# Kernel tuning notes

Measured on AMD Instinct MI355X. Metric: run time of the kernel, lower is better.

The kernel has to match this reference:

```python
import jax, jax.numpy as jnp
import numpy as np

B, D, H, C, HALT_H, MAX_STEPS = 8192, 2048, 1024, 1000, 32, 10
EPS = 1e-08


def setup_inputs() -> dict:
    key = jax.random.key(0)
    ks = jax.random.split(key, 12)
    s = 0.02
    return {
        "x": jax.random.normal(ks[0], (B, D), jnp.float32),
        "enc_W": jax.random.normal(ks[1], (H, D), jnp.float32) * s,
        "enc_b": jnp.zeros((H,), jnp.float32),
        "ln_g": jnp.ones((H,), jnp.float32),
        "ln_b": jnp.zeros((H,), jnp.float32),
        "W_ih": jax.random.normal(ks[2], (3 * H, H), jnp.float32) * s,
        "W_hh": jax.random.normal(ks[3], (3 * H, H), jnp.float32) * s,
        "b_ih": jnp.zeros((3 * H,), jnp.float32),
        "b_hh": jnp.zeros((3 * H,), jnp.float32),
        "cls_W": jax.random.normal(ks[4], (C, H), jnp.float32) * s,
        "cls_b": jnp.zeros((C,), jnp.float32),
        "h1_W": jax.random.normal(ks[5], (HALT_H, H), jnp.float32) * s,
        "h1_b": jnp.zeros((HALT_H,), jnp.float32),
        "h2_W": jax.random.normal(ks[6], (1, HALT_H), jnp.float32) * s,
        "h2_b": jnp.zeros((1,), jnp.float32),
    }


def _forward(x, enc_W, enc_b, ln_g, ln_b, W_ih, W_hh, b_ih, b_hh,
             cls_W, cls_b, h1_W, h1_b, h2_W, h2_b):
    # encoder: Linear -> LayerNorm -> GELU (exact)
    z = x @ enc_W.T + enc_b
    mu = jnp.mean(z, axis=-1, keepdims=True)
    var = jnp.var(z, axis=-1, keepdims=True)
    z = (z - mu) * jax.lax.rsqrt(var + 1e-05) * ln_g + ln_b
    h0 = jax.nn.gelu(z, approximate=False)

    def step(h, _):
        gi = h @ W_ih.T + b_ih   # GRUCell with input = hidden
        gh = h @ W_hh.T + b_hh
        gi_r, gi_z, gi_n = jnp.split(gi, 3, axis=-1)
        gh_r, gh_z, gh_n = jnp.split(gh, 3, axis=-1)
        r = jax.nn.sigmoid(gi_r + gh_r)
        zt = jax.nn.sigmoid(gi_z + gh_z)
        n = jnp.tanh(gi_n + r * gh_n)
        h_new = (1.0 - zt) * n + zt * h
        logits = h_new @ cls_W.T + cls_b                         # [B, C]
        halt = jax.nn.sigmoid(
            jax.nn.relu(h_new @ h1_W.T + h1_b) @ h2_W.T + h2_b
        )[:, 0]                                                   # [B]
        return h_new, (logits, halt)

    _, (logits_steps, halt_steps) = jax.lax.scan(step, h0, None, length=MAX_STEPS)
    logits_stack = jnp.transpose(logits_steps, (1, 0, 2))  # [B, T, C]
    halts_stack = jnp.transpose(halt_steps, (1, 0))        # [B, T]

    log_not_halt = jnp.log(1.0 - halts_stack + EPS)
    cumsum_log = jnp.cumsum(log_not_halt, axis=1)
    cumsum_shifted = jnp.concatenate(
        [jnp.zeros((halts_stack.shape[0], 1), halts_stack.dtype), cumsum_log[:, :-1]], axis=1)
    halt_dist = halts_stack * jnp.exp(cumsum_shifted)
    remainder = 1.0 - jnp.sum(halt_dist, axis=1, keepdims=True)
    halt_dist = jnp.concatenate(
        [halt_dist[:, :-1], halt_dist[:, -1:] + jnp.maximum(remainder, 0.0)], axis=1)

    weighted_logits = jnp.sum(halt_dist[:, :, None] * logits_stack, axis=1)  # [B, C]
    step_indices = jnp.arange(1, MAX_STEPS + 1, dtype=weighted_logits.dtype)
    expected_steps = jnp.sum(halt_dist * step_indices, axis=1)
    probs = jax.nn.softmax(weighted_logits, axis=1)
    softmax_conf = jnp.max(probs, axis=1)
    comp_uncertainty = expected_steps / MAX_STEPS
    confidence = 0.7 * softmax_conf + 0.3 * (1.0 - comp_uncertainty)
    return (weighted_logits, probs, confidence, softmax_conf,
            expected_steps, halt_dist, comp_uncertainty)


def reference(x, enc_W, enc_b, ln_g, ln_b, W_ih, W_hh, b_ih, b_hh,
              cls_W, cls_b, h1_W, h1_b, h2_W, h2_b):
    return _forward(x, enc_W, enc_b, ln_g, ln_b, W_ih, W_hh, b_ih, b_hh,
                    cls_W, cls_b, h1_W, h1_b, h2_W, h2_b)
```

## Files before the change

### kernel.cpp

```cpp
#include <hip/hip_runtime.h>
#include <hip/hip_bf16.h>

#define B_ 8192
#define D_ 2048
#define H_ 1024
#define C_ 1000
#define NSTEP 10

typedef __attribute__((ext_vector_type(8))) short short8;
typedef __attribute__((ext_vector_type(4))) float f32x4;

__device__ __forceinline__ f32x4 mfma16x16(short8 a, short8 b, f32x4 c) {
  return __builtin_amdgcn_mfma_f32_16x16x32_bf16(a, b, c, 0, 0, 0);
}

__device__ __forceinline__ void async16(void* lds_uniform, const void* gsrc) {
  __builtin_amdgcn_global_load_lds(
      (const __attribute__((address_space(1))) void*)gsrc,
      (__attribute__((address_space(3))) void*)lds_uniform, 16, 0, 0);
}

__device__ __forceinline__ float sigm(float x) { return 1.0f / (1.0f + __expf(-x)); }
__device__ __forceinline__ float tanh_fast(float x) { return 1.0f - 2.0f / (__expf(2.0f * x) + 1.0f); }
__device__ __forceinline__ float b2f(short s) {
  union { unsigned u; float f; } v; v.u = ((unsigned)(unsigned short)s) << 16; return v.f;
}
__device__ __forceinline__ unsigned short f2us(float f) {
  __hip_bfloat16 h = __float2bfloat16(f); return *(unsigned short*)&h;
}

__device__ __forceinline__ int swz(int row, int slot) {
  return (row << 7) + (((slot) ^ (row & 7)) << 4);
}

__global__ void cvt_bf16_pad(const float* __restrict__ src, __hip_bfloat16* __restrict__ dst,
                             int n4, int nsrc4) {
  int i = blockIdx.x * 256 + threadIdx.x;
  if (i >= n4) return;
  float4 v = make_float4(0.f, 0.f, 0.f, 0.f);
  if (i < nsrc4) v = ((const float4*)src)[i];
  ((ushort4*)dst)[i] = make_ushort4(f2us(v.x), f2us(v.y), f2us(v.z), f2us(v.w));
}

__global__ void cvt_gates(const float* __restrict__ Wih, const float* __restrict__ Whh,
                          __hip_bfloat16* __restrict__ dst) {
  const int i = blockIdx.x * 256 + threadIdx.x;
  const int per_gate = (H_ * H_) / 4;
  const int gate = i / per_gate, rem = i - gate * per_gate;
  float4 v;
  if (gate == 0) {
    float4 a = ((const float4*)Wih)[rem], b = ((const float4*)Whh)[rem];
    v = make_float4(a.x + b.x, a.y + b.y, a.z + b.z, a.w + b.w);
  } else if (gate == 1) {
    float4 a = ((const float4*)Wih)[per_gate + rem], b = ((const float4*)Whh)[per_gate + rem];
    v = make_float4(a.x + b.x, a.y + b.y, a.z + b.z, a.w + b.w);
  } else if (gate == 2) {
    v = ((const float4*)Wih)[2 * per_gate + rem];
  } else {
    v = ((const float4*)Whh)[2 * per_gate + rem];
  }
  ((ushort4*)dst)[i] = make_ushort4(f2us(v.x), f2us(v.y), f2us(v.z), f2us(v.w));
}

template<int EPI>
__global__ __launch_bounds__(256, 2)
void gemm_bt(const __hip_bfloat16* __restrict__ A, int lda,
             const __hip_bfloat16* __restrict__ Bt, int ldb, int K,
             const float* __restrict__ bias,
             float* __restrict__ out, int out_ld, int ncol,
             const float* __restrict__ wrow) {
  __shared__ __hip_bfloat16 sA[128 * 64];
  __shared__ __hip_bfloat16 sB[128 * 64];
  const int tid = threadIdx.x;
  const int wave = tid >> 6, lane = tid & 63;
  const int m0 = blockIdx.x * 128, n0 = blockIdx.y * 128;
  const int wm = (wave >> 1) * 64, wn = (wave & 1) * 64;
  const int lr = lane & 15;
  const int g4 = lane >> 4;
  const int srow = wave * 8 + (lane >> 3);
  const int scol = ((lane & 7) ^ ((lane >> 3) & 7)) * 8;

  f32x4 acc[4][4] = {};

  const __hip_bfloat16* Asrc = A + (size_t)(m0 + srow) * lda + scol;
  const __hip_bfloat16* Bsrc = Bt + (size_t)(n0 + srow) * ldb + scol;

  for (int k0 = 0; k0 < K; k0 += 64) {
#pragma unroll
    for (int c = 0; c < 4; ++c) {
      async16((char*)sA + c * 4096 + wave * 1024, Asrc + (size_t)(c * 32) * lda + k0);
      async16((char*)sB + c * 4096 + wave * 1024, Bsrc + (size_t)(c * 32) * ldb + k0);
    }
    __syncthreads();
#pragma unroll
    for (int ks = 0; ks < 2; ++ks) {
      const int slot = ks * 4 + g4;
      short8 af[4], bfr[4];
#pragma unroll
      for (int i = 0; i < 4; ++i) {
        af[i]  = *(const short8*)((const char*)sA + swz(wm + i * 16 + lr, slot));
        bfr[i] = *(const short8*)((const char*)sB + swz(wn + i * 16 + lr, slot));
      }
#pragma unroll
      for (int i = 0; i < 4; ++i)
#pragma unroll
        for (int j = 0; j < 4; ++j)
          acc[i][j] = mfma16x16(af[i], bfr[j], acc[i][j]);
    }
    __syncthreads();
  }

  const int rbase = (lane >> 4) * 4;
  const int cbase = lane & 15;
#pragma unroll
  for (int i = 0; i < 4; ++i) {
#pragma unroll
    for (int r = 0; r < 4; ++r) {
      const int grow = m0 + wm + i * 16 + rbase + r;
      if (EPI == 1) {
        const float ws = wrow[grow];
#pragma unroll
        for (int j = 0; j < 4; ++j) {
          const int gcol = n0 + wn + j * 16 + cbase;
          if (gcol < ncol)
            out[(size_t)grow * out_ld + gcol] = acc[i][j][r] + bias[gcol] * ws;
        }
      } else {
#pragma unroll
        for (int j = 0; j < 4; ++j) {
          const int gcol = n0 + wn + j * 16 + cbase;
          out[(size_t)grow * out_ld + gcol] = acc[i][j][r] + bias[gcol];
        }
      }
    }
  }
}

__global__ __launch_bounds__(256, 2)
void gemm_gru(const __hip_bfloat16* __restrict__ A,
              const __hip_bfloat16* __restrict__ Wc4,
              const float* __restrict__ b_ih, const float* __restrict__ b_hh,
              __hip_bfloat16* __restrict__ hnewb) {
  __shared__ __hip_bfloat16 sA[128 * 64];
  __shared__ __hip_bfloat16 sB[4 * 64 * 64];
  const int tid = threadIdx.x, wave = tid >> 6, lane = tid & 63;
  const int m0 = blockIdx.x * 128, n0 = blockIdx.y * 64;
  const int wr = wave >> 1, wc = wave & 1;
  const int lr = lane & 15;
  const int g4 = lane >> 4;
  const int srow = lane >> 3;
  const int scol = ((lane & 7) ^ ((lane >> 3) & 7)) * 8;

  f32x4 acc[4][4][2] = {};

  const __hip_bfloat16* Asrc = A + (size_t)(m0 + wave * 8 + srow) * H_ + scol;
  const __hip_bfloat16* Bsrc = Wc4 + (size_t)(n0 + wave * 8 + srow) * H_ + scol;

  for (int k0 = 0; k0 < H_; k0 += 64) {
#pragma unroll
    for (int c = 0; c < 4; ++c)
      async16((char*)sA + c * 4096 + wave * 1024, Asrc + (size_t)(c * 32) * H_ + k0);
#pragma unroll
    for (int g = 0; g < 4; ++g)
#pragma unroll
      for (int d = 0; d < 2; ++d)
        async16((char*)sB + g * 8192 + d * 4096 + wave * 1024,
                Bsrc + ((size_t)g << 20) + (size_t)(d * 32) * H_ + k0);
    __syncthreads();
#pragma unroll
    for (int ks = 0; ks < 2; ++ks) {
      const int slot = ks * 4 + g4;
      short8 af[4];
#pragma unroll
      for (int mi = 0; mi < 4; ++mi)
        af[mi] = *(const short8*)((const char*)sA + swz(wr * 64 + mi * 16 + lr, slot));
      short8 bf[4][2];
#pragma unroll
      for (int g = 0; g < 4; ++g)
#pragma unroll
        for (int hb = 0; hb < 2; ++hb)
          bf[g][hb] = *(const short8*)((const char*)sB + g * 8192
                                       + swz(wc * 32 + hb * 16 + lr, slot));
#pragma unroll
      for (int mi = 0; mi < 4; ++mi)
#pragma unroll
        for (int g = 0; g < 4; ++g)
#pragma unroll
          for (int hb = 0; hb < 2; ++hb)
            acc[mi][g][hb] = mfma16x16(af[mi], bf[g][hb], acc[mi][g][hb]);
    }
    __syncthreads();
  }

  const int rbase = (lane >> 4) * 4;
  const int cbase = lane & 15;
#pragma unroll
  for (int hb = 0; hb < 2; ++hb) {
    const int gcol = n0 + wc * 32 + hb * 16 + cbase;
    const float brz = b_ih[gcol] + b_hh[gcol];
    const float bzz = b_ih[H_ + gcol] + b_hh[H_ + gcol];
    const float bin = b_ih[2 * H_ + gcol];
    const float bhn = b_hh[2 * H_ + gcol];
#pragma unroll
    for (int mi = 0; mi < 4; ++mi) {
#pragma unroll
      for (int r = 0; r < 4; ++r) {
        const int grow = m0 + wr * 64 + mi * 16 + rbase + r;
        const size_t idx = (size_t)grow * H_ + gcol;
        const float rg = sigm(acc[mi][0][hb][r] + brz);
        const float zg = sigm(acc[mi][1][hb][r] + bzz);
        const float ng = tanh_fast(acc[mi][2][hb][r] + bin + rg * (acc[mi][3][hb][r] + bhn));
        const float hv = b2f(*(const short*)(A + idx));
        hnewb[idx] = __float2bfloat16((1.0f - zg) * ng + zg * hv);
      }
    }
  }
}

__global__ void ln_gelu(const float* __restrict__ z, const float* __restrict__ g,
                        const float* __restrict__ bta, __hip_bfloat16* __restrict__ hb) {
  const int row = blockIdx.x, t = threadIdx.x;
  __shared__ float rs[4], rs2[4];
  float4 v = ((const float4*)(z + (size_t)row * H_))[t];
  float s = v.x + v.y + v.z + v.w;
  float s2 = v.x * v.x + v.y * v.y + v.z * v.z + v.w * v.w;
#pragma unroll
  for (int off = 32; off; off >>= 1) {
    s += __shfl_down(s, off);
    s2 += __shfl_down(s2, off);
  }
  if ((t & 63) == 0) { rs[t >> 6] = s; rs2[t >> 6] = s2; }
  __syncthreads();
  const float mu = (rs[0] + rs[1] + rs[2] + rs[3]) * (1.0f / H_);
  const float var = (rs2[0] + rs2[1] + rs2[2] + rs2[3]) * (1.0f / H_) - mu * mu;
  const float rstd = rsqrtf(var + 1e-5f);
  float4 gg = ((const float4*)g)[t];
  float4 bb = ((const float4*)bta)[t];
  float o[4], res[4];
  o[0] = (v.x - mu) * rstd * gg.x + bb.x;
  o[1] = (v.y - mu) * rstd * gg.y + bb.y;
  o[2] = (v.z - mu) * rstd * gg.z + bb.z;
  o[3] = (v.w - mu) * rstd * gg.w + bb.w;
#pragma unroll
  for (int k = 0; k < 4; ++k)
    res[k] = 0.5f * o[k] * (1.0f + erff(o[k] * 0.70710678118654752f));
  ((ushort4*)(hb + (size_t)row * H_))[t] =
      make_ushort4(f2us(res[0]), f2us(res[1]), f2us(res[2]), f2us(res[3]));
}

__global__ __launch_bounds__(256, 4)
void halt_mlp_all(const __hip_bfloat16* __restrict__ hstack,
                  const __hip_bfloat16* __restrict__ h1Wb,
                  const float* __restrict__ h1b, const float* __restrict__ h2W,
                  const float* __restrict__ h2b,
                  float* __restrict__ hbuf) {
  __shared__ float part[2][2][64][8];
  const int tid = threadIdx.x, wave = tid >> 6, lane = tid & 63;
  const int tstep = blockIdx.y;
  const __hip_bfloat16* hb = hstack + (size_t)(tstep + 1) * B_ * H_;
  const int rowgrp = wave >> 1, khalf = wave & 1;
  const int m0 = (blockIdx.x * 2 + rowgrp) * 16;
  const int lr = lane & 15, lk = (lane >> 4) * 8;

  const __hip_bfloat16* Arow = hb + (size_t)(m0 + lr) * H_ + khalf * 512 + lk;
  const __hip_bfloat16* B0 = h1Wb + (size_t)lr * H_ + khalf * 512 + lk;
  const __hip_bfloat16* B1 = h1Wb + (size_t)(16 + lr) * H_ + khalf * 512 + lk;
  f32x4 acc0 = {}, acc1 = {};
#pragma unroll 4
  for (int kk = 0; kk < 512; kk += 32) {
    short8 a  = *(const short8*)(Arow + kk);
    short8 b0 = *(const short8*)(B0 + kk);
    short8 b1 = *(const short8*)(B1 + kk);
    acc0 = mfma16x16(a, b0, acc0);
    acc1 = mfma16x16(a, b1, acc1);
  }
#pragma unroll
  for (int q = 0; q < 4; ++q) {
    part[rowgrp][khalf][lane][q]     = acc0[q];
    part[rowgrp][khalf][lane][4 + q] = acc1[q];
  }
  __syncthreads();
  if (khalf) return;

  const float w2a = h2W[lr], w2b = h2W[16 + lr];
  const float b1a = h1b[lr], b1b = h1b[16 + lr];
  float p[4];
#pragma unroll
  for (int q = 0; q < 4; ++q) {
    const float u0 = part[rowgrp][0][lane][q]     + part[rowgrp][1][lane][q]     + b1a;
    const float u1 = part[rowgrp][0][lane][4 + q] + part[rowgrp][1][lane][4 + q] + b1b;
    p[q] = fmaxf(u0, 0.f) * w2a + fmaxf(u1, 0.f) * w2b;
  }
#pragma unroll
  for (int m = 1; m < 16; m <<= 1) {
#pragma unroll
    for (int q = 0; q < 4; ++q) p[q] += __shfl_xor(p[q], m);
  }
  if (lr == 0) {
    const float b2 = h2b[0];
#pragma unroll
    for (int q = 0; q < 4; ++q) {
      const int row = m0 + (lane >> 4) * 4 + q;
      hbuf[(size_t)row * NSTEP + tstep] = 1.f / (1.f + expf(-(p[q] + b2)));
    }
  }
}

__global__ void ponder_rec(const float* __restrict__ hbuf,
                           float* __restrict__ out_hd, float* __restrict__ out_es,
                           float* __restrict__ out_cu, float* __restrict__ wsum) {
  const int row = blockIdx.x * 256 + threadIdx.x;
  const float* hp = hbuf + (size_t)row * NSTEP;
  float c = 0.f, ps = 0.f, es = 0.f;
  float hd[NSTEP];
#pragma unroll
  for (int t = 0; t < NSTEP; ++t) {
    const float halt = hp[t];
    const float pt = halt * expf(c);
    float w;
    if (t == NSTEP - 1) {
      w = pt + fmaxf(1.f - (ps + pt), 0.f);
    } else {
      w = pt;
      c += logf(1.f - halt + 1e-8f);
      ps += pt;
    }
    es += w * (float)(t + 1);
    hd[t] = w;
  }
#pragma unroll
  for (int t = 0; t < NSTEP; ++t) out_hd[(size_t)row * NSTEP + t] = hd[t];
  out_es[row] = es;
  out_cu[row] = es * (1.0f / NSTEP);
  wsum[row] = ps + hd[NSTEP - 1];
}

__global__ void hw_final(const __hip_bfloat16* __restrict__ hstack,
                         const float* __restrict__ out_hd,
                         __hip_bfloat16* __restrict__ hwb) {
  const int t = threadIdx.x;
  const int row = blockIdx.x * 4 + (t >> 6);
  const int c0 = (t & 63) * 16;
  const float* hd = out_hd + (size_t)row * NSTEP;
  float accv[16] = {};
#pragma unroll
  for (int s = 0; s < NSTEP; ++s) {
    const float w = hd[s];
    const short8* p = (const short8*)(hstack + ((size_t)(s + 1) * B_ + row) * H_ + c0);
    short8 a0 = p[0], a1 = p[1];
#pragma unroll
    for (int q = 0; q < 8; ++q) accv[q] += w * b2f(a0[q]);
#pragma unroll
    for (int q = 0; q < 8; ++q) accv[8 + q] += w * b2f(a1[q]);
  }
  short8 r0, r1;
#pragma unroll
  for (int q = 0; q < 8; ++q) { r0[q] = (short)f2us(accv[q]); r1[q] = (short)f2us(accv[8 + q]); }
  short8* dst = (short8*)(hwb + (size_t)row * H_ + c0);
  dst[0] = r0; dst[1] = r1;
}

__global__ void finalize(const float* __restrict__ wl, const float* __restrict__ es,
                         float* __restrict__ probs, float* __restrict__ conf,
                         float* __restrict__ sconf) {
  const int row = blockIdx.x, t = threadIdx.x;
  __shared__ float red[4], red2[4];
  float4 v = make_float4(-1e30f, -1e30f, -1e30f, -1e30f);
  float m = -1e30f;
  if (t < 250) {
    v = ((const float4*)(wl + (size_t)row * C_))[t];
    m = fmaxf(fmaxf(v.x, v.y), fmaxf(v.z, v.w));
  }
#pragma unroll
  for (int off = 32; off; off >>= 1) m = fmaxf(m, __shfl_down(m, off));
  if ((t & 63) == 0) red[t >> 6] = m;
  __syncthreads();
  m = fmaxf(fmaxf(red[0], red[1]), fmaxf(red[2], red[3]));
  float4 e = make_float4(0.f, 0.f, 0.f, 0.f);
  float s = 0.f;
  if (t < 250) {
    e.x = expf(v.x - m); e.y = expf(v.y - m); e.z = expf(v.z - m); e.w = expf(v.w - m);
    s = e.x + e.y + e.z + e.w;
  }
#pragma unroll
  for (int off = 32; off; off >>= 1) s += __shfl_down(s, off);
  if ((t & 63) == 0) red2[t >> 6] = s;
  __syncthreads();
  s = red2[0] + red2[1] + red2[2] + red2[3];
  const float inv = 1.0f / s;
  if (t < 250)
    ((float4*)(probs + (size_t)row * C_))[t] = make_float4(e.x * inv, e.y * inv, e.z * inv, e.w * inv);
  if (t == 0) {
    sconf[row] = inv;
    conf[row] = 0.7f * inv + 0.3f * (1.0f - es[row] * (1.0f / NSTEP));
  }
}

extern "C" void kernel_launch(void* const* d_in, const int* in_sizes, int n_in,
                              void* d_out, int out_size, void* d_ws, size_t ws_size,
                              hipStream_t stream) {
  (void)in_sizes; (void)n_in; (void)out_size; (void)ws_size;
  const float* x     = (const float*)d_in[0];
  const float* enc_W = (const float*)d_in[1];
  const float* enc_b = (const float*)d_in[2];
  const float* ln_g  = (const float*)d_in[3];
  const float* ln_b  = (const float*)d_in[4];
  const float* W_ih  = (const float*)d_in[5];
  const float* W_hh  = (const float*)d_in[6];
  const float* b_ih  = (const float*)d_in[7];
  const float* b_hh  = (const float*)d_in[8];
  const float* cls_W = (const float*)d_in[9];
  const float* cls_b = (const float*)d_in[10];
  const float* h1_W  = (const float*)d_in[11];
  const float* h1_b  = (const float*)d_in[12];
  const float* h2_W  = (const float*)d_in[13];
  const float* h2_b  = (const float*)d_in[14];

  char* wsp = (char*)d_ws;
  auto carve = [&](size_t n) { char* p = wsp; wsp += (n + 255) & ~(size_t)255; return p; };
  __hip_bfloat16* Wc4b   = (__hip_bfloat16*)carve((size_t)4 * H_ * H_ * 2);
  __hip_bfloat16* clsWb  = (__hip_bfloat16*)carve((size_t)1024 * 1024 * 2);
  __hip_bfloat16* encWb  = (__hip_bfloat16*)carve((size_t)H_ * D_ * 2);
  __hip_bfloat16* h1Wb   = (__hip_bfloat16*)carve((size_t)32 * H_ * 2);
  __hip_bfloat16* hstack = (__hip_bfloat16*)carve((size_t)(NSTEP + 1) * B_ * H_ * 2);
  float* wsum = (float*)carve((size_t)B_ * 4);
  float* hbuf = (float*)carve((size_t)B_ * NSTEP * 4);

  const size_t SLOT = (size_t)B_ * H_;
  float* z            = (float*)(hstack + SLOT);
  __hip_bfloat16* xb  = hstack + 3 * SLOT;
  __hip_bfloat16* hwb = hstack;

  float* out = (float*)d_out;
  float* out_wl    = out;
  float* out_probs = out + (size_t)B_ * C_;
  float* out_conf  = out + (size_t)2 * B_ * C_;
  float* out_sconf = out_conf + B_;
  float* out_es    = out_sconf + B_;
  float* out_hd    = out_es + B_;
  float* out_cu    = out_hd + (size_t)B_ * NSTEP;

  dim3 blk(256);
  { int n4 = B_ * D_ / 4;       cvt_bf16_pad<<<(n4 + 255) / 256, blk, 0, stream>>>(x, xb, n4, n4); }
  { int n4 = H_ * D_ / 4;       cvt_bf16_pad<<<(n4 + 255) / 256, blk, 0, stream>>>(enc_W, encWb, n4, n4); }
  { int n4 = 4 * H_ * H_ / 4;   cvt_gates<<<(n4 + 255) / 256, blk, 0, stream>>>(W_ih, W_hh, Wc4b); }
  { int n4 = 1024 * 1024 / 4;   cvt_bf16_pad<<<(n4 + 255) / 256, blk, 0, stream>>>(cls_W, clsWb, n4, C_ * H_ / 4); }
  { int n4 = 32 * H_ / 4;       cvt_bf16_pad<<<(n4 + 255) / 256, blk, 0, stream>>>(h1_W, h1Wb, n4, n4); }

  gemm_bt<0><<<dim3(B_ / 128, H_ / 128), blk, 0, stream>>>(
      xb, D_, encWb, D_, D_, enc_b, z, H_, H_, nullptr);
  ln_gelu<<<B_, blk, 0, stream>>>(z, ln_g, ln_b, hstack);

  for (int step = 0; step < NSTEP; ++step) {
    const __hip_bfloat16* hprev = hstack + (size_t)step * SLOT;
    __hip_bfloat16* hnext = hstack + (size_t)(step + 1) * SLOT;
    gemm_gru<<<dim3(B_ / 128, H_ / 64), blk, 0, stream>>>(
        hprev, Wc4b, b_ih, b_hh, hnext);
  }

  halt_mlp_all<<<dim3(B_ / 32, NSTEP), blk, 0, stream>>>(
      hstack, h1Wb, h1_b, h2_W, h2_b, hbuf);
  ponder_rec<<<B_ / 256, blk, 0, stream>>>(hbuf, out_hd, out_es, out_cu, wsum);

  hw_final<<<B_ / 4, blk, 0, stream>>>(hstack, out_hd, hwb);

  gemm_bt<1><<<dim3(B_ / 128, 1024 / 128), blk, 0, stream>>>(
      hwb, H_, clsWb, H_, H_, cls_b, out_wl, C_, C_, wsum);

  finalize<<<B_, blk, 0, stream>>>(out_wl, out_es, out_probs, out_conf, out_sconf);
}
```

Measured before the change: 907.5 us.

## Overlap halt MLP with GRU steps and merge weight conversion kernels

The halting MLP for step t-1 now runs inside the GRU kernel for step t, using an extra grid column (blockIdx.y==16) that reads the previous hidden state. Only the final step needs a separate halt_last kernel. The five fp32-to-bf16 conversion launches are merged into one cvt_all kernel that dispatches on the flat index. The aim is to hide the halt MLP's memory reads behind GRU GEMM work and to cut launch overhead, at the cost of a slightly uneven grid and extra branching.

```diff
diff --git a/kernel.cpp b/kernel.cpp
--- a/kernel.cpp
+++ b/kernel.cpp
@@ -33,33 +33,108 @@
   return (row << 7) + (((slot) ^ (row & 7)) << 4);
 }
 
-__global__ void cvt_bf16_pad(const float* __restrict__ src, __hip_bfloat16* __restrict__ dst,
-                             int n4, int nsrc4) {
-  int i = blockIdx.x * 256 + threadIdx.x;
-  if (i >= n4) return;
-  float4 v = make_float4(0.f, 0.f, 0.f, 0.f);
-  if (i < nsrc4) v = ((const float4*)src)[i];
-  ((ushort4*)dst)[i] = make_ushort4(f2us(v.x), f2us(v.y), f2us(v.z), f2us(v.w));
-}
-
-__global__ void cvt_gates(const float* __restrict__ Wih, const float* __restrict__ Whh,
-                          __hip_bfloat16* __restrict__ dst) {
+__device__ __forceinline__ void halt_rows32(
+    const __hip_bfloat16* __restrict__ hb, const __hip_bfloat16* __restrict__ h1Wb,
+    const float* __restrict__ h1b, const float* __restrict__ h2W,
+    const float* __restrict__ h2b, float* __restrict__ hbuf, int tcol,
+    int m0base, float (*part)[2][64][8]) {
+  const int tid = threadIdx.x, wave = tid >> 6, lane = tid & 63;
+  const int rowgrp = wave >> 1, khalf = wave & 1;
+  const int m0 = m0base + rowgrp * 16;
+  const int lr = lane & 15, lk = (lane >> 4) * 8;
+
+  const __hip_bfloat16* Arow = hb + (size_t)(m0 + lr) * H_ + khalf * 512 + lk;
+  const __hip_bfloat16* B0 = h1Wb + (size_t)lr * H_ + khalf * 512 + lk;
+  const __hip_bfloat16* B1 = h1Wb + (size_t)(16 + lr) * H_ + khalf * 512 + lk;
+  f32x4 acc0 = {}, acc1 = {};
+#pragma unroll 4
+  for (int kk = 0; kk < 512; kk += 32) {
+    short8 a  = *(const short8*)(Arow + kk);
+    short8 b0 = *(const short8*)(B0 + kk);
+    short8 b1 = *(const short8*)(B1 + kk);
+    acc0 = mfma16x16(a, b0, acc0);
+    acc1 = mfma16x16(a, b1, acc1);
+  }
+#pragma unroll
+  for (int q = 0; q < 4; ++q) {
+    part[rowgrp][khalf][lane][q]     = acc0[q];
+    part[rowgrp][khalf][lane][4 + q] = acc1[q];
+  }
+  __syncthreads();
+  if (!khalf) {
+    const float w2a = h2W[lr], w2b = h2W[16 + lr];
+    const float b1a = h1b[lr], b1b = h1b[16 + lr];
+    float p[4];
+#pragma unroll
+    for (int q = 0; q < 4; ++q) {
+      const float u0 = part[rowgrp][0][lane][q]     + part[rowgrp][1][lane][q]     + b1a;
+      const float u1 = part[rowgrp][0][lane][4 + q] + part[rowgrp][1][lane][4 + q] + b1b;
+      p[q] = fmaxf(u0, 0.f) * w2a + fmaxf(u1, 0.f) * w2b;
+    }
+#pragma unroll
+    for (int m = 1; m < 16; m <<= 1) {
+#pragma unroll
+      for (int q = 0; q < 4; ++q) p[q] += __shfl_xor(p[q], m);
+    }
+    if (lr == 0) {
+      const float b2 = h2b[0];
+#pragma unroll
+      for (int q = 0; q < 4; ++q) {
+        const int row = m0 + (lane >> 4) * 4 + q;
+        hbuf[(size_t)row * NSTEP + tcol] = 1.f / (1.f + expf(-(p[q] + b2)));
+      }
+    }
+  }
+  __syncthreads();
+}
+
+__global__ void cvt_all(const float* __restrict__ x, const float* __restrict__ encW,
+                        const float* __restrict__ Wih, const float* __restrict__ Whh,
+                        const float* __restrict__ clsW, const float* __restrict__ h1W,
+                        __hip_bfloat16* __restrict__ xb, __hip_bfloat16* __restrict__ encWb,
+                        __hip_bfloat16* __restrict__ Wc4b, __hip_bfloat16* __restrict__ clsWb,
+                        __hip_bfloat16* __restrict__ h1Wb) {
   const int i = blockIdx.x * 256 + threadIdx.x;
-  const int per_gate = (H_ * H_) / 4;
-  const int gate = i / per_gate, rem = i - gate * per_gate;
+  const int b0 = B_ * D_ / 4;
+  const int b1 = b0 + H_ * D_ / 4;
+  const int b2 = b1 + H_ * H_;
+  const int b3 = b2 + 1024 * 1024 / 4;
+  const int b4 = b3 + 32 * H_ / 4;
+  if (i >= b4) return;
   float4 v;
-  if (gate == 0) {
-    float4 a = ((const float4*)Wih)[rem], b = ((const float4*)Whh)[rem];
-    v = make_float4(a.x + b.x, a.y + b.y, a.z + b.z, a.w + b.w);
-  } else if (gate == 1) {
-    float4 a = ((const float4*)Wih)[per_gate + rem], b = ((const float4*)Whh)[per_gate + rem];
-    v = make_float4(a.x + b.x, a.y + b.y, a.z + b.z, a.w + b.w);
-  } else if (gate == 2) {
-    v = ((const float4*)Wih)[2 * per_gate + rem];
+  __hip_bfloat16* dst;
+  int di;
+  if (i < b0) {
+    v = ((const float4*)x)[i]; dst = xb; di = i;
+  } else if (i < b1) {
+    const int j = i - b0;
+    v = ((const float4*)encW)[j]; dst = encWb; di = j;
+  } else if (i < b2) {
+    const int j = i - b1;
+    const int per_gate = H_ * H_ / 4;
+    const int gate = j / per_gate, rem = j - gate * per_gate;
+    if (gate == 0) {
+      float4 a = ((const float4*)Wih)[rem], b = ((const float4*)Whh)[rem];
+      v = make_float4(a.x + b.x, a.y + b.y, a.z + b.z, a.w + b.w);
+    } else if (gate == 1) {
+      float4 a = ((const float4*)Wih)[per_gate + rem], b = ((const float4*)Whh)[per_gate + rem];
+      v = make_float4(a.x + b.x, a.y + b.y, a.z + b.z, a.w + b.w);
+    } else if (gate == 2) {
+      v = ((const float4*)Wih)[2 * per_gate + rem];
+    } else {
+      v = ((const float4*)Whh)[2 * per_gate + rem];
+    }
+    dst = Wc4b; di = j;
+  } else if (i < b3) {
+    const int j = i - b2;
+    v = make_float4(0.f, 0.f, 0.f, 0.f);
+    if (j < C_ * H_ / 4) v = ((const float4*)clsW)[j];
+    dst = clsWb; di = j;
   } else {
-    v = ((const float4*)Whh)[2 * per_gate + rem];
-  }
-  ((ushort4*)dst)[i] = make_ushort4(f2us(v.x), f2us(v.y), f2us(v.z), f2us(v.w));
+    const int j = i - b3;
+    v = ((const float4*)h1W)[j]; dst = h1Wb; di = j;
+  }
+  ((ushort4*)dst)[di] = make_ushort4(f2us(v.x), f2us(v.y), f2us(v.z), f2us(v.w));
 }
 
 template<int EPI>
@@ -140,9 +215,22 @@
 void gemm_gru(const __hip_bfloat16* __restrict__ A,
               const __hip_bfloat16* __restrict__ Wc4,
               const float* __restrict__ b_ih, const float* __restrict__ b_hh,
-              __hip_bfloat16* __restrict__ hnewb) {
+              __hip_bfloat16* __restrict__ hnewb,
+              const __hip_bfloat16* __restrict__ h1Wb,
+              const float* __restrict__ h1b, const float* __restrict__ h2W,
+              const float* __restrict__ h2b, float* __restrict__ hbuf, int tcol) {
   __shared__ __hip_bfloat16 sA[128 * 64];
   __shared__ __hip_bfloat16 sB[4 * 64 * 64];
+  if (blockIdx.y == 16) {
+    if (tcol >= 0) {
+      float (*part)[2][64][8] = (float (*)[2][64][8])sA;
+      const int band = blockIdx.x * 128;
+#pragma unroll
+      for (int c = 0; c < 4; ++c)
+        halt_rows32(A, h1Wb, h1b, h2W, h2b, hbuf, tcol, band + c * 32, part);
+    }
+    return;
+  }
   const int tid = threadIdx.x, wave = tid >> 6, lane = tid & 63;
   const int m0 = blockIdx.x * 128, n0 = blockIdx.y * 64;
   const int wr = wave >> 1, wc = wave & 1;
@@ -215,6 +303,15 @@
       }
     }
   }
+}
+
+__global__ __launch_bounds__(256, 4)
+void halt_last(const __hip_bfloat16* __restrict__ hb,
+               const __hip_bfloat16* __restrict__ h1Wb,
+               const float* __restrict__ h1b, const float* __restrict__ h2W,
+               const float* __restrict__ h2b, float* __restrict__ hbuf, int tcol) {
+  __shared__ float part[2][2][64][8];
+  halt_rows32(hb, h1Wb, h1b, h2W, h2b, hbuf, tcol, blockIdx.x * 32, part);
 }
 
 __global__ void ln_gelu(const float* __restrict__ z, const float* __restrict__ g,
@@ -246,64 +343,6 @@
     res[k] = 0.5f * o[k] * (1.0f + erff(o[k] * 0.70710678118654752f));
   ((ushort4*)(hb + (size_t)row * H_))[t] =
       make_ushort4(f2us(res[0]), f2us(res[1]), f2us(res[2]), f2us(res[3]));
-}
-
-__global__ __launch_bounds__(256, 4)
-void halt_mlp_all(const __hip_bfloat16* __restrict__ hstack,
-                  const __hip_bfloat16* __restrict__ h1Wb,
-                  const float* __restrict__ h1b, const float* __restrict__ h2W,
-                  const float* __restrict__ h2b,
-                  float* __restrict__ hbuf) {
-  __shared__ float part[2][2][64][8];
-  const int tid = threadIdx.x, wave = tid >> 6, lane = tid & 63;
-  const int tstep = blockIdx.y;
-  const __hip_bfloat16* hb = hstack + (size_t)(tstep + 1) * B_ * H_;
-  const int rowgrp = wave >> 1, khalf = wave & 1;
-  const int m0 = (blockIdx.x * 2 + rowgrp) * 16;
-  const int lr = lane & 15, lk = (lane >> 4) * 8;
-
-  const __hip_bfloat16* Arow = hb + (size_t)(m0 + lr) * H_ + khalf * 512 + lk;
-  const __hip_bfloat16* B0 = h1Wb + (size_t)lr * H_ + khalf * 512 + lk;
-  const __hip_bfloat16* B1 = h1Wb + (size_t)(16 + lr) * H_ + khalf * 512 + lk;
-  f32x4 acc0 = {}, acc1 = {};
-#pragma unroll 4
-  for (int kk = 0; kk < 512; kk += 32) {
-    short8 a  = *(const short8*)(Arow + kk);
-    short8 b0 = *(const short8*)(B0 + kk);
-    short8 b1 = *(const short8*)(B1 + kk);
-    acc0 = mfma16x16(a, b0, acc0);
-    acc1 = mfma16x16(a, b1, acc1);
-  }
-#pragma unroll
-  for (int q = 0; q < 4; ++q) {
-    part[rowgrp][khalf][lane][q]     = acc0[q];
-    part[rowgrp][khalf][lane][4 + q] = acc1[q];
-  }
-  __syncthreads();
-  if (khalf) return;
-
-  const float w2a = h2W[lr], w2b = h2W[16 + lr];
-  const float b1a = h1b[lr], b1b = h1b[16 + lr];
-  float p[4];
-#pragma unroll
-  for (int q = 0; q < 4; ++q) {
-    const float u0 = part[rowgrp][0][lane][q]     + part[rowgrp][1][lane][q]     + b1a;
-    const float u1 = part[rowgrp][0][lane][4 + q] + part[rowgrp][1][lane][4 + q] + b1b;
-    p[q] = fmaxf(u0, 0.f) * w2a + fmaxf(u1, 0.f) * w2b;
-  }
-#pragma unroll
-  for (int m = 1; m < 16; m <<= 1) {
-#pragma unroll
-    for (int q = 0; q < 4; ++q) p[q] += __shfl_xor(p[q], m);
-  }
-  if (lr == 0) {
-    const float b2 = h2b[0];
-#pragma unroll
-    for (int q = 0; q < 4; ++q) {
-      const int row = m0 + (lane >> 4) * 4 + q;
-      hbuf[(size_t)row * NSTEP + tstep] = 1.f / (1.f + expf(-(p[q] + b2)));
-    }
-  }
 }
 
 __global__ void ponder_rec(const float* __restrict__ hbuf,
@@ -441,11 +480,11 @@
   float* out_cu    = out_hd + (size_t)B_ * NSTEP;
 
   dim3 blk(256);
-  { int n4 = B_ * D_ / 4;       cvt_bf16_pad<<<(n4 + 255) / 256, blk, 0, stream>>>(x, xb, n4, n4); }
-  { int n4 = H_ * D_ / 4;       cvt_bf16_pad<<<(n4 + 255) / 256, blk, 0, stream>>>(enc_W, encWb, n4, n4); }
-  { int n4 = 4 * H_ * H_ / 4;   cvt_gates<<<(n4 + 255) / 256, blk, 0, stream>>>(W_ih, W_hh, Wc4b); }
-  { int n4 = 1024 * 1024 / 4;   cvt_bf16_pad<<<(n4 + 255) / 256, blk, 0, stream>>>(cls_W, clsWb, n4, C_ * H_ / 4); }
-  { int n4 = 32 * H_ / 4;       cvt_bf16_pad<<<(n4 + 255) / 256, blk, 0, stream>>>(h1_W, h1Wb, n4, n4); }
+  {
+    const int total = B_ * D_ / 4 + H_ * D_ / 4 + H_ * H_ + 1024 * 1024 / 4 + 32 * H_ / 4;
+    cvt_all<<<(total + 255) / 256, blk, 0, stream>>>(
+        x, enc_W, W_ih, W_hh, cls_W, h1_W, xb, encWb, Wc4b, clsWb, h1Wb);
+  }
 
   gemm_bt<0><<<dim3(B_ / 128, H_ / 128), blk, 0, stream>>>(
       xb, D_, encWb, D_, D_, enc_b, z, H_, H_, nullptr);
@@ -454,12 +493,12 @@
   for (int step = 0; step < NSTEP; ++step) {
     const __hip_bfloat16* hprev = hstack + (size_t)step * SLOT;
     __hip_bfloat16* hnext = hstack + (size_t)(step + 1) * SLOT;
-    gemm_gru<<<dim3(B_ / 128, H_ / 64), blk, 0, stream>>>(
-        hprev, Wc4b, b_ih, b_hh, hnext);
-  }
-
-  halt_mlp_all<<<dim3(B_ / 32, NSTEP), blk, 0, stream>>>(
-      hstack, h1Wb, h1_b, h2_W, h2_b, hbuf);
+    gemm_gru<<<dim3(B_ / 128, 17), blk, 0, stream>>>(
+        hprev, Wc4b, b_ih, b_hh, hnext, h1Wb, h1_b, h2_W, h2_b, hbuf, step - 1);
+  }
+  halt_last<<<B_ / 32, blk, 0, stream>>>(
+      hstack + (size_t)NSTEP * SLOT, h1Wb, h1_b, h2_W, h2_b, hbuf, NSTEP - 1);
+
   ponder_rec<<<B_ / 256, blk, 0, stream>>>(hbuf, out_hd, out_es, out_cu, wsum);
 
   hw_final<<<B_ / 4, blk, 0, stream>>>(hstack, out_hd, hwb);
```

Result: slower. 1.058 ms (+16.6%).
